# Optimization experiments

Measured on AMD Instinct MI355X. Metric: run time of the kernel, lower is better.

## Reference

```python
import jax, jax.numpy as jnp
import numpy as np

VOCAB, EMB, HID, LAYERS = 23, 16, 256, 8


def _lstm_layer(xseq, Wih, Whh, bih, bhh):
    # xseq: [B,T,D_in]; Wih: [4H,D_in]; Whh: [4H,H]; biases: [4H]
    B = xseq.shape[0]
    H = Whh.shape[1]
    # precompute input contribution to gates for all timesteps
    xg = jnp.einsum('btd,gd->btg', xseq, Wih) + bih + bhh  # [B,T,4H]
    xg = jnp.swapaxes(xg, 0, 1)  # [T,B,4H] for scan

    def step(carry, g_in):
        h, c = carry
        g = g_in + h @ Whh.T  # [B,4H]
        i, f, gg, o = jnp.split(g, 4, axis=-1)  # PyTorch gate order i,f,g,o
        i = jax.nn.sigmoid(i)
        f = jax.nn.sigmoid(f)
        gg = jnp.tanh(gg)
        o = jax.nn.sigmoid(o)
        c = f * c + i * gg
        h = o * jnp.tanh(c)
        return (h, c), h

    h0 = jnp.zeros((B, H), xseq.dtype)
    c0 = jnp.zeros((B, H), xseq.dtype)
    (_, _), hs = jax.lax.scan(step, (h0, c0), xg)
    return jnp.swapaxes(hs, 0, 1)  # [B,T,H]


def setup_inputs() -> dict:
    key = jax.random.key(0)
    ks = jax.random.split(key, 8)
    B, T = 64, 512
    s_e = 1.0 / np.sqrt(HID)
    x = jax.random.randint(ks[0], (B, T), 0, VOCAB)
    emb = jax.random.normal(ks[1], (VOCAB, EMB), jnp.float32)
    W_ih0 = jax.random.uniform(ks[2], (4 * HID, EMB), jnp.float32, -s_e, s_e)
    W_ih_rest = jax.random.uniform(ks[3], (LAYERS - 1, 4 * HID, HID), jnp.float32, -s_e, s_e)
    W_hh = jax.random.uniform(ks[4], (LAYERS, 4 * HID, HID), jnp.float32, -s_e, s_e)
    b_ih = jax.random.uniform(ks[5], (LAYERS, 4 * HID), jnp.float32, -s_e, s_e)
    b_hh = jax.random.uniform(ks[6], (LAYERS, 4 * HID), jnp.float32, -s_e, s_e)
    fc_w = jax.random.uniform(ks[7], (VOCAB, HID), jnp.float32, -s_e, s_e)
    fc_b = jnp.zeros((VOCAB,), jnp.float32)
    return {"x": x, "emb": emb, "W_ih0": W_ih0, "W_ih_rest": W_ih_rest,
            "W_hh": W_hh, "b_ih": b_ih, "b_hh": b_hh, "fc_w": fc_w, "fc_b": fc_b}


def reference(x, emb, W_ih0, W_ih_rest, W_hh, b_ih, b_hh, fc_w, fc_b):
    h = emb[x]  # [B,T,EMB]
    h = _lstm_layer(h, W_ih0, W_hh[0], b_ih[0], b_hh[0])
    for l in range(1, LAYERS):
        h = _lstm_layer(h, W_ih_rest[l - 1], W_hh[l], b_ih[l], b_hh[l])
    return h @ fc_w.T + fc_b  # [B,T,VOCAB]
```

## Files before the change

kernel.cpp:

```cpp
#include <hip/hip_runtime.h>
#include <cstdint>
#include <cstddef>

#define BB   64
#define TT   512
#define HH   256
#define G4   1024
#define NL   8
#define NW   32
#define HPW  8
#define NR   32

#define POLL_BOUND (1 << 15)

typedef _Float16 half8 __attribute__((ext_vector_type(8)));
typedef float   floatx4 __attribute__((ext_vector_type(4)));

__device__ __forceinline__ float sigm(float v)   { return 1.0f / (1.0f + __expf(-v)); }
__device__ __forceinline__ float tanh_f(float v) { return 1.0f - 2.0f / (__expf(2.0f * v) + 1.0f); }

__device__ __forceinline__ void gstore8_x(_Float16* p, half8 d) {
  asm volatile("global_store_dwordx4 %0, %1, off sc0 sc1" :: "v"(p), "v"(d) : "memory");
}
__device__ __forceinline__ void stdword_x(int* p, int v) {
  asm volatile("global_store_dword %0, %1, off sc0 sc1" :: "v"(p), "v"(v) : "memory");
}
__device__ __forceinline__ void wait_vm0() {
  asm volatile("s_waitcnt vmcnt(0)" ::: "memory");
}
__device__ __forceinline__ int ldflag_x(const int* p) {
  int v; asm volatile("global_load_dword %0, %1, off sc0 sc1" : "=v"(v) : "v"(p) : "memory");
  wait_vm0(); return v;
}

#define TSTRIDE ((size_t)32 * BB * 8)
#define LSTRIDE ((size_t)TT * TSTRIDE)

__global__ void build_xg0(const float* __restrict__ emb, const float* __restrict__ Wih0,
                          float* __restrict__ table) {
  int i = blockIdx.x * 256 + threadIdx.x;
  if (i >= 23 * G4) return;
  int v = i >> 10, n = i & (G4 - 1);
  float a = 0.f;
#pragma unroll
  for (int e = 0; e < 16; ++e) a += emb[v * 16 + e] * Wih0[n * 16 + e];
  table[i] = a;
}

__global__ __launch_bounds__(256, 1) void lstm_pipeline(
    const int*   __restrict__ x,
    const float* __restrict__ Wih_rest,
    const float* __restrict__ Whh,
    const float* __restrict__ bih,
    const float* __restrict__ bhh,
    const float* __restrict__ xg0t,
    _Float16* __restrict__ hseq,
    int* __restrict__ cnt)
{
  const int l   = blockIdx.x & 7;
  const int w   = blockIdx.x >> 3;
  const int tid = threadIdx.x;
  const int lane = tid & 63;
  const int p    = tid >> 6;

  __shared__ __align__(16) _Float16 wlds[64 * NR * 8];
  __shared__ __align__(16) _Float16 hl[BB * 8];
  __shared__ float  blds[NR];
  __shared__ float  tlds[23 * NR];

  for (int idx = tid; idx < 64 * NR; idx += 256) {
    int kc = idx >> 5;
    int n  = idx & 31;
    int g = n >> 3, jl = n & 7;
    int gr = g * 256 + w * HPW + jl;
    float v[8];
    if (kc < 32) {
      if (l == 0) { for (int j = 0; j < 8; ++j) v[j] = 0.f; }
      else {
        const float* src = Wih_rest + ((size_t)(l - 1) * G4 + gr) * HH + kc * 8;
        for (int j = 0; j < 8; ++j) v[j] = src[j];
      }
    } else {
      const float* src = Whh + ((size_t)l * G4 + gr) * HH + (kc - 32) * 8;
      for (int j = 0; j < 8; ++j) v[j] = src[j];
    }
    _Float16* dst = wlds + (size_t)idx * 8;
    for (int j = 0; j < 8; ++j) dst[j] = (_Float16)v[j];
  }
  if (tid < NR) {
    int g = tid >> 3, jl = tid & 7;
    int gr = g * 256 + w * HPW + jl;
    blds[tid] = bih[l * G4 + gr] + bhh[l * G4 + gr];
  }
  if (l == 0) {
    for (int idx = tid; idx < 23 * NR; idx += 256) {
      int v = idx >> 5, n = idx & 31;
      int g = n >> 3, jl = n & 7;
      tlds[idx] = xg0t[v * G4 + g * 256 + w * HPW + jl];
    }
  }
  if (tid == 0) (void)__hip_atomic_load(cnt, __ATOMIC_ACQUIRE, __HIP_MEMORY_SCOPE_AGENT);
  __syncthreads();

  const int arow = p * 16 + (lane & 15);
  const int kq   = lane >> 4;
  const int n0   = lane & 15;
  const int n1   = 16 + n0;
  const int cu   = lane & 7;
  const bool lowh = (n0 < 8);
  const int roff = lowh ? 0 : 2;
  const int rowb = p * 16 + kq * 4;

  const _Float16* hin  = hseq + (size_t)(l > 0 ? l - 1 : 0) * LSTRIDE;
  _Float16*       hrec = hseq + (size_t)l * LSTRIDE;

  const float bi = blds[cu], bf = blds[8 + cu], bg = blds[16 + cu], bo = blds[24 + cu];

  float cst[2] = {0.f, 0.f};

  for (int t = 0; t < TT; ++t) {
    floatx4 acc0 = {0.f, 0.f, 0.f, 0.f};
    floatx4 acc1 = {0.f, 0.f, 0.f, 0.f};

    if (l > 0 && t > 0) {
      const _Float16* ain = hin + (size_t)t * TSTRIDE;
      half8 aA[8];
#pragma unroll
      for (int kt = 0; kt < 8; ++kt) {
        int kc = kt * 4 + kq;
        aA[kt] = *(const half8*)(ain + ((size_t)(kc * 64 + arow) << 3));
      }
#pragma unroll
      for (int kt = 0; kt < 8; ++kt) {
        int kc = kt * 4 + kq;
        half8 w0 = *(const half8*)(wlds + ((kc * 32 + n0) << 3));
        half8 w1 = *(const half8*)(wlds + ((kc * 32 + n1) << 3));
        acc0 = __builtin_amdgcn_mfma_f32_16x16x32_f16(aA[kt], w0, acc0, 0, 0, 0);
        acc1 = __builtin_amdgcn_mfma_f32_16x16x32_f16(aA[kt], w1, acc1, 0, 0, 0);
      }
    }

    if (t > 0 && p == 3) {
      const int* f = cnt + l * NW;
      for (int it = 0; it < POLL_BOUND; ++it) {
        int v = ldflag_x(f + (lane & 31));
        if (__all(v >= t)) break;
        __builtin_amdgcn_s_sleep(1);
      }
    }
    if (l > 0 && p == 2) {
      const int tgt = (t + 2 < TT) ? t + 2 : TT;
      const int* f = cnt + (l - 1) * NW;
      for (int it = 0; it < POLL_BOUND; ++it) {
        int v = ldflag_x(f + (lane & 31));
        if (__all(v >= tgt)) break;
        __builtin_amdgcn_s_sleep(1);
      }
    }
    __syncthreads();

    if (l > 0 && t == 0) {
      const _Float16* ain = hin;
      half8 aA[8];
#pragma unroll
      for (int kt = 0; kt < 8; ++kt) {
        int kc = kt * 4 + kq;
        aA[kt] = *(const half8*)(ain + ((size_t)(kc * 64 + arow) << 3));
      }
#pragma unroll
      for (int kt = 0; kt < 8; ++kt) {
        int kc = kt * 4 + kq;
        half8 w0 = *(const half8*)(wlds + ((kc * 32 + n0) << 3));
        half8 w1 = *(const half8*)(wlds + ((kc * 32 + n1) << 3));
        acc0 = __builtin_amdgcn_mfma_f32_16x16x32_f16(aA[kt], w0, acc0, 0, 0, 0);
        acc1 = __builtin_amdgcn_mfma_f32_16x16x32_f16(aA[kt], w1, acc1, 0, 0, 0);
      }
    }

    if (t > 0) {
      const _Float16* ain = hrec + (size_t)(t - 1) * TSTRIDE;
      half8 aB[8];
#pragma unroll
      for (int kt = 0; kt < 8; ++kt) {
        int kc = kt * 4 + kq;
        aB[kt] = *(const half8*)(ain + ((size_t)(kc * 64 + arow) << 3));
      }
#pragma unroll
      for (int kt = 0; kt < 8; ++kt) {
        int kc = kt * 4 + kq;
        half8 w0 = *(const half8*)(wlds + (((32 + kc) * 32 + n0) << 3));
        half8 w1 = *(const half8*)(wlds + (((32 + kc) * 32 + n1) << 3));
        acc0 = __builtin_amdgcn_mfma_f32_16x16x32_f16(aB[kt], w0, acc0, 0, 0, 0);
        acc1 = __builtin_amdgcn_mfma_f32_16x16x32_f16(aB[kt], w1, acc1, 0, 0, 0);
      }
    }

    const float sa0 = lowh ? acc0[2] : acc0[0];
    const float sa1 = lowh ? acc0[3] : acc0[1];
    const float sb0 = lowh ? acc1[2] : acc1[0];
    const float sb1 = lowh ? acc1[3] : acc1[1];
    const float ra0 = __shfl_xor(sa0, 8);
    const float ra1 = __shfl_xor(sa1, 8);
    const float rb0 = __shfl_xor(sb0, 8);
    const float rb1 = __shfl_xor(sb1, 8);

#pragma unroll
    for (int rr = 0; rr < 2; ++rr) {
      const int r = roff + rr;
      const float own0 = acc0[r], own1 = acc1[r];
      const float oth0 = rr ? ra1 : ra0;
      const float oth1 = rr ? rb1 : rb0;
      float gi = (lowh ? own0 : oth0) + bi;
      float gf = (lowh ? oth0 : own0) + bf;
      float gg = (lowh ? own1 : oth1) + bg;
      float go = (lowh ? oth1 : own1) + bo;
      if (l == 0) {
        const int xv = x[(rowb + r) * TT + t];
        const float* tb = tlds + xv * NR;
        gi += tb[cu]; gf += tb[8 + cu]; gg += tb[16 + cu]; go += tb[24 + cu];
      }
      const float iv = sigm(gi), fv = sigm(gf), gv = tanh_f(gg), ov = sigm(go);
      cst[rr] = fv * cst[rr] + iv * gv;
      const float hv = ov * tanh_f(cst[rr]);
      hl[(rowb + r) * 8 + cu] = (_Float16)hv;
    }
    __syncthreads();

    if (tid < 64) {
      __builtin_amdgcn_s_setprio(1);
      half8 hv = *(const half8*)(hl + tid * 8);
      gstore8_x(hrec + (size_t)t * TSTRIDE + ((size_t)(w * 64 + tid) << 3), hv);
      wait_vm0();
      if (tid == 0)
        stdword_x(cnt + l * NW + w, t + 1);
      __builtin_amdgcn_s_setprio(0);
    }
  }
}

__global__ __launch_bounds__(256) void fc_kernel(
    const _Float16* __restrict__ hseq7,
    const float* __restrict__ fcw,
    const float* __restrict__ fcb,
    float* __restrict__ out)
{
  const int t = blockIdx.x;
  const int tid = threadIdx.x;
  const int lane = tid & 63;
  const int p = tid >> 6;

  __shared__ __align__(16) _Float16 whi[32 * 32 * 8];
  __shared__ __align__(16) _Float16 wlo[32 * 32 * 8];
  __shared__ float bbuf[32];

  for (int idx = tid; idx < 32 * 32; idx += 256) {
    int kc = idx >> 5, n = idx & 31;
    _Float16* dh = whi + (size_t)idx * 8;
    _Float16* dl = wlo + (size_t)idx * 8;
    if (n < 23) {
      const float* src = fcw + n * 256 + kc * 8;
      for (int j = 0; j < 8; ++j) {
        float v = src[j];
        _Float16 hi = (_Float16)v;
        dh[j] = hi;
        dl[j] = (_Float16)((v - (float)hi) * 2048.0f);
      }
    } else {
      for (int j = 0; j < 8; ++j) { dh[j] = (_Float16)0.f; dl[j] = (_Float16)0.f; }
    }
  }
  if (tid < 32) bbuf[tid] = (tid < 23) ? fcb[tid] : 0.f;
  __syncthreads();

  const int arow = p * 16 + (lane & 15);
  const int kq   = lane >> 4;
  const int n0   = lane & 15;
  const int n1   = 16 + n0;

  const _Float16* src = hseq7 + (size_t)t * TSTRIDE;
  floatx4 a0h = {0.f,0.f,0.f,0.f}, a1h = {0.f,0.f,0.f,0.f};
  floatx4 a0l = {0.f,0.f,0.f,0.f}, a1l = {0.f,0.f,0.f,0.f};
#pragma unroll
  for (int kt = 0; kt < 8; ++kt) {
    int kc = kt * 4 + kq;
    half8 a  = *(const half8*)(src + ((size_t)(kc * 64 + arow) << 3));
    half8 h0 = *(const half8*)(whi + ((kc * 32 + n0) << 3));
    half8 h1 = *(const half8*)(whi + ((kc * 32 + n1) << 3));
    half8 l0 = *(const half8*)(wlo + ((kc * 32 + n0) << 3));
    half8 l1 = *(const half8*)(wlo + ((kc * 32 + n1) << 3));
    a0h = __builtin_amdgcn_mfma_f32_16x16x32_f16(a, h0, a0h, 0, 0, 0);
    a1h = __builtin_amdgcn_mfma_f32_16x16x32_f16(a, h1, a1h, 0, 0, 0);
    a0l = __builtin_amdgcn_mfma_f32_16x16x32_f16(a, l0, a0l, 0, 0, 0);
    a1l = __builtin_amdgcn_mfma_f32_16x16x32_f16(a, l1, a1l, 0, 0, 0);
  }

  const float rs = 1.0f / 2048.0f;
#pragma unroll
  for (int r = 0; r < 4; ++r) {
    int b = p * 16 + kq * 4 + r;
    out[((size_t)b * TT + t) * 23 + n0] = a0h[r] + a0l[r] * rs + bbuf[n0];
    if (n1 < 23)
      out[((size_t)b * TT + t) * 23 + n1] = a1h[r] + a1l[r] * rs + bbuf[n1];
  }
}

extern "C" void kernel_launch(void* const* d_in, const int* in_sizes, int n_in,
                              void* d_out, int out_size, void* d_ws, size_t ws_size,
                              hipStream_t stream) {
  const int*   x        = (const int*)d_in[0];
  const float* emb      = (const float*)d_in[1];
  const float* Wih0     = (const float*)d_in[2];
  const float* Wih_rest = (const float*)d_in[3];
  const float* Whh      = (const float*)d_in[4];
  const float* bihp     = (const float*)d_in[5];
  const float* bhhp     = (const float*)d_in[6];
  const float* fcw      = (const float*)d_in[7];
  const float* fcb      = (const float*)d_in[8];
  float* out = (float*)d_out;

  char* ws = (char*)d_ws;
  int*      cnt   = (int*)ws;
  float*    table = (float*)(ws + 16384);
  _Float16* hseq  = (_Float16*)(ws + 131072);

  hipMemsetAsync(ws, 0, 16384, stream);
  build_xg0<<<(23 * G4 + 255) / 256, 256, 0, stream>>>(emb, Wih0, table);
  lstm_pipeline<<<NL * NW, 256, 0, stream>>>(x, Wih_rest, Whh, bihp, bhhp, table, hseq, cnt);
  fc_kernel<<<TT, 256, 0, stream>>>(hseq + (size_t)7 * LSTRIDE, fcw, fcb, out);
}
```

Measured before the change: 1.602 ms.

## Poll recurrent hidden-state data for sentinels instead of per-step flag handshakes

The hidden-state buffer is pre-filled with a NaN byte pattern (0x7F7F7F7F). The recurrent read then spins on the loaded h(t-1) tiles themselves, reloading only the chunks that still hold the sentinel. This replaces the old sequence of store, wait for completion, write a counter flag, then have another wave poll that flag. It is meant to take one global-memory round trip off the critical path of each serial timestep. The cost is an extra memset over the whole multi-layer hidden-state buffer every call, and the cross-layer counter is now published when a wave reads its inputs rather than after its store completes.

```diff
diff --git a/kernel.cpp b/kernel.cpp
--- a/kernel.cpp
+++ b/kernel.cpp
@@ -13,8 +13,11 @@
 
 #define POLL_BOUND (1 << 15)
 
+#define SENT 0x7F7F7F7F
+
 typedef _Float16 half8 __attribute__((ext_vector_type(8)));
 typedef float   floatx4 __attribute__((ext_vector_type(4)));
+typedef int     intx4  __attribute__((ext_vector_type(4)));
 
 __device__ __forceinline__ float sigm(float v)   { return 1.0f / (1.0f + __expf(-v)); }
 __device__ __forceinline__ float tanh_f(float v) { return 1.0f - 2.0f / (__expf(2.0f * v) + 1.0f); }
@@ -31,6 +34,11 @@
 __device__ __forceinline__ int ldflag_x(const int* p) {
   int v; asm volatile("global_load_dword %0, %1, off sc0 sc1" : "=v"(v) : "v"(p) : "memory");
   wait_vm0(); return v;
+}
+__device__ __forceinline__ intx4 ld16_x(const _Float16* p) {
+  intx4 v;
+  asm volatile("global_load_dwordx4 %0, %1, off sc0 sc1" : "=v"(v) : "v"(p) : "memory");
+  return v;
 }
 
 #define TSTRIDE ((size_t)32 * BB * 8)
@@ -140,14 +148,6 @@
       }
     }
 
-    if (t > 0 && p == 3) {
-      const int* f = cnt + l * NW;
-      for (int it = 0; it < POLL_BOUND; ++it) {
-        int v = ldflag_x(f + (lane & 31));
-        if (__all(v >= t)) break;
-        __builtin_amdgcn_s_sleep(1);
-      }
-    }
     if (l > 0 && p == 2) {
       const int tgt = (t + 2 < TT) ? t + 2 : TT;
       const int* f = cnt + (l - 1) * NW;
@@ -179,19 +179,40 @@
 
     if (t > 0) {
       const _Float16* ain = hrec + (size_t)(t - 1) * TSTRIDE;
-      half8 aB[8];
-#pragma unroll
-      for (int kt = 0; kt < 8; ++kt) {
-        int kc = kt * 4 + kq;
-        aB[kt] = *(const half8*)(ain + ((size_t)(kc * 64 + arow) << 3));
-      }
-#pragma unroll
-      for (int kt = 0; kt < 8; ++kt) {
-        int kc = kt * 4 + kq;
+      const _Float16* ap[8];
+      intx4 raw[8];
+#pragma unroll
+      for (int kt = 0; kt < 8; ++kt) {
+        int kc = kt * 4 + kq;
+        ap[kt]  = ain + ((size_t)(kc * 64 + arow) << 3);
+        raw[kt] = ld16_x(ap[kt]);
+      }
+      wait_vm0();
+      __builtin_amdgcn_sched_barrier(0);
+      if (tid == 0) stdword_x(cnt + l * NW + w, t);
+      for (int it = 0; it < POLL_BOUND; ++it) {
+        int bad = 0;
+#pragma unroll
+        for (int kt = 0; kt < 8; ++kt) {
+          const intx4 r = raw[kt];
+          const int b = (r.x == SENT) | (r.y == SENT) | (r.z == SENT) | (r.w == SENT);
+          bad |= b << kt;
+        }
+        if (!__any(bad != 0)) break;
+#pragma unroll
+        for (int kt = 0; kt < 8; ++kt)
+          if (bad & (1 << kt)) raw[kt] = ld16_x(ap[kt]);
+        wait_vm0();
+        __builtin_amdgcn_sched_barrier(0);
+      }
+#pragma unroll
+      for (int kt = 0; kt < 8; ++kt) {
+        int kc = kt * 4 + kq;
+        union { intx4 i; half8 h; } u; u.i = raw[kt];
         half8 w0 = *(const half8*)(wlds + (((32 + kc) * 32 + n0) << 3));
         half8 w1 = *(const half8*)(wlds + (((32 + kc) * 32 + n1) << 3));
-        acc0 = __builtin_amdgcn_mfma_f32_16x16x32_f16(aB[kt], w0, acc0, 0, 0, 0);
-        acc1 = __builtin_amdgcn_mfma_f32_16x16x32_f16(aB[kt], w1, acc1, 0, 0, 0);
+        acc0 = __builtin_amdgcn_mfma_f32_16x16x32_f16(u.h, w0, acc0, 0, 0, 0);
+        acc1 = __builtin_amdgcn_mfma_f32_16x16x32_f16(u.h, w1, acc1, 0, 0, 0);
       }
     }
 
@@ -230,11 +251,13 @@
       __builtin_amdgcn_s_setprio(1);
       half8 hv = *(const half8*)(hl + tid * 8);
       gstore8_x(hrec + (size_t)t * TSTRIDE + ((size_t)(w * 64 + tid) << 3), hv);
-      wait_vm0();
-      if (tid == 0)
-        stdword_x(cnt + l * NW + w, t + 1);
       __builtin_amdgcn_s_setprio(0);
     }
+  }
+
+  if (tid < 64) {
+    wait_vm0();
+    if (tid == 0) stdword_x(cnt + l * NW + w, TT);
   }
 }
 
@@ -324,6 +347,7 @@
   _Float16* hseq  = (_Float16*)(ws + 131072);
 
   hipMemsetAsync(ws, 0, 16384, stream);
+  hipMemsetAsync(ws + 131072, 0x7F, (size_t)NL * LSTRIDE * sizeof(_Float16), stream);
   build_xg0<<<(23 * G4 + 255) / 256, 256, 0, stream>>>(emb, Wih0, table);
   lstm_pipeline<<<NL * NW, 256, 0, stream>>>(x, Wih_rest, Whh, bihp, bhhp, table, hseq, cnt);
   fc_kernel<<<TT, 256, 0, stream>>>(hseq + (size_t)7 * LSTRIDE, fcw, fcb, out);
```

Result: slower. 1.690 ms (+5.5%).
